# Kernel tuning notes

Hardware: AMD Instinct MI355X
Metric: run time of the kernel (lower is better)

Reference implementation:

```python
import jax, jax.numpy as jnp
import numpy as np

D = 1024

def setup_inputs() -> dict:
    key = jax.random.key(0)
    kx, kw = jax.random.split(key)
    x = jax.random.normal(kx, (4, 2048, D), dtype=jnp.float32)
    # nn.Linear(d, 3d, bias=False): weight [3d, d]; y = x @ W.T
    W = jax.random.normal(kw, (3 * D, D), dtype=jnp.float32) * (1.0 / np.sqrt(D))
    return {"x": x, "W": W}

def reference(x, W):
    d = x.shape[-1]
    qkv = jnp.einsum('bsd,ed->bse', x, W)  # [B,S,3d]
    q, k, v = jnp.split(qkv, 3, axis=2)
    att = jnp.einsum('bqd,bkd->bqk', q, k) * (1.0 / jnp.sqrt(jnp.asarray(d, x.dtype)))
    att = jax.nn.softmax(att, axis=-1)
    y = jnp.einsum('bqk,bkd->bqd', att, v)
    return y
```

## Files before the change

kernel.cpp:

```cpp
#include <hip/hip_runtime.h>
#include <hip/hip_bf16.h>

typedef __attribute__((ext_vector_type(8))) short short8;
typedef __attribute__((ext_vector_type(4))) float f32x4;

typedef unsigned short u16;

__device__ __forceinline__ u16 f32_to_bf16(float f) {
    unsigned int u = __float_as_uint(f);
    u += 0x7fffu + ((u >> 16) & 1u);
    return (u16)(u >> 16);
}

__device__ __forceinline__ void gload16(const u16* g, u16* lds_base) {
    __builtin_amdgcn_global_load_lds(
        (const __attribute__((address_space(1))) void*)g,
        (__attribute__((address_space(3))) void*)lds_base, 16, 0, 0);
}

__global__ void cast_inputs(const float* __restrict__ x, u16* __restrict__ Xb,
                            const float* __restrict__ W, u16* __restrict__ Wb,
                            int nx4, int nw4) {
    int i = blockIdx.x * blockDim.x + threadIdx.x;
    const float* in; u16* out; int idx;
    if (i < nx4) { in = x; out = Xb; idx = i; }
    else { idx = i - nx4; if (idx >= nw4) return; in = W; out = Wb; }
    float4 v = ((const float4*)in)[idx];
    ushort4 o;
    o.x = f32_to_bf16(v.x); o.y = f32_to_bf16(v.y);
    o.z = f32_to_bf16(v.z); o.w = f32_to_bf16(v.w);
    ((ushort4*)out)[idx] = o;
}


struct Frag128 { f32x4 acc[4][4]; int lane, wm, wn; };

__device__ __forceinline__ void gemm_core_128(
    const u16* __restrict__ A, const u16* __restrict__ Bt, int K, int lda, int ldb,
    int row0, int col0, u16* sA, u16* sB, Frag128& fr)
{
    const int t    = threadIdx.x;
    const int lane = t & 63;
    const int wave = t >> 6;
    fr.lane = lane;
    fr.wm = (wave >> 1) * 64;
    fr.wn = (wave & 1) * 64;
    const int lr = lane & 15;

#pragma unroll
    for (int i = 0; i < 4; ++i)
#pragma unroll
        for (int j = 0; j < 4; ++j)
            fr.acc[i][j] = (f32x4){0.f, 0.f, 0.f, 0.f};

    const int srow = lane >> 3;
    const int gc   = (lane & 7) ^ srow;
    for (int k0 = 0; k0 < K; k0 += 64) {
        __syncthreads();
#pragma unroll
        for (int c = 0; c < 4; ++c) {
            const int rb = c * 32 + wave * 8;
            const int r  = rb + srow;
            gload16(A  + (long long)(row0 + r) * lda + k0 + gc * 8, &sA[rb * 64]);
            gload16(Bt + (long long)(col0 + r) * ldb + k0 + gc * 8, &sB[rb * 64]);
        }
        __syncthreads();

#pragma unroll
        for (int kk = 0; kk < 64; kk += 32) {
            const int cb = (lane >> 4) + (kk >> 3);
            const int sl = (cb ^ (lr & 7)) * 8;
            short8 af[4], bf[4];
#pragma unroll
            for (int i = 0; i < 4; ++i) {
                af[i] = *(const short8*)(&sA[(fr.wm + i * 16 + lr) * 64 + sl]);
                bf[i] = *(const short8*)(&sB[(fr.wn + i * 16 + lr) * 64 + sl]);
            }
#pragma unroll
            for (int i = 0; i < 4; ++i)
#pragma unroll
                for (int j = 0; j < 4; ++j)
                    fr.acc[i][j] = __builtin_amdgcn_mfma_f32_16x16x32_bf16(
                        af[i], bf[j], fr.acc[i][j], 0, 0, 0);
        }
    }
}

struct FragN64 { f32x4 acc[2][4]; int lane, wm; };

__device__ __forceinline__ void gemm_core_n64(
    const u16* __restrict__ A, const u16* __restrict__ Bt, int K, int lda, int ldb,
    int row0, int col0, u16* sA, u16* sB, FragN64& fr)
{
    const int t    = threadIdx.x;
    const int lane = t & 63;
    const int wave = t >> 6;
    fr.lane = lane;
    fr.wm = wave * 32;
    const int lr = lane & 15;

#pragma unroll
    for (int i = 0; i < 2; ++i)
#pragma unroll
        for (int j = 0; j < 4; ++j)
            fr.acc[i][j] = (f32x4){0.f, 0.f, 0.f, 0.f};

    const int srow = lane >> 3;
    const int gc   = (lane & 7) ^ srow;
    for (int k0 = 0; k0 < K; k0 += 64) {
        __syncthreads();
#pragma unroll
        for (int c = 0; c < 4; ++c) {
            const int rb = c * 32 + wave * 8;
            gload16(A + (long long)(row0 + rb + srow) * lda + k0 + gc * 8,
                    &sA[rb * 64]);
        }
#pragma unroll
        for (int c = 0; c < 2; ++c) {
            const int rb = c * 32 + wave * 8;
            gload16(Bt + (long long)(col0 + rb + srow) * ldb + k0 + gc * 8,
                    &sB[rb * 64]);
        }
        __syncthreads();

#pragma unroll
        for (int kk = 0; kk < 64; kk += 32) {
            const int cb = (lane >> 4) + (kk >> 3);
            const int sl = (cb ^ (lr & 7)) * 8;
            short8 af[2], bf[4];
#pragma unroll
            for (int i = 0; i < 2; ++i)
                af[i] = *(const short8*)(&sA[(fr.wm + i * 16 + lr) * 64 + sl]);
#pragma unroll
            for (int j = 0; j < 4; ++j)
                bf[j] = *(const short8*)(&sB[(j * 16 + lr) * 64 + sl]);
#pragma unroll
            for (int i = 0; i < 2; ++i)
#pragma unroll
                for (int j = 0; j < 4; ++j)
                    fr.acc[i][j] = __builtin_amdgcn_mfma_f32_16x16x32_bf16(
                        af[i], bf[j], fr.acc[i][j], 0, 0, 0);
        }
    }
}


__global__ __launch_bounds__(256) void gemm_qkv(
    const u16* __restrict__ Xb, const u16* __restrict__ Wb,
    u16* __restrict__ QK, u16* __restrict__ VT)
{
    __shared__ u16 smem[2 * 128 * 64];
    u16* sA = smem;
    u16* sB = smem + 128 * 64;
    const int row0 = blockIdx.y * 128;

    if (blockIdx.x < 16) {
        const int col0 = blockIdx.x * 128;
        Frag128 fr;
        gemm_core_128(Xb, Wb, 1024, 1024, 1024, row0, col0, sA, sB, fr);
        const int cr = (fr.lane >> 4) * 4, cc = fr.lane & 15;
#pragma unroll
        for (int i = 0; i < 4; ++i)
#pragma unroll
            for (int j = 0; j < 4; ++j)
#pragma unroll
                for (int r = 0; r < 4; ++r) {
                    int grow = row0 + fr.wm + i * 16 + cr + r;
                    int gcol = col0 + fr.wn + j * 16 + cc;
                    QK[(long long)grow * 2048 + gcol] = f32_to_bf16(fr.acc[i][j][r]);
                }
    } else {
        const int col0 = (blockIdx.x - 16) * 64;
        FragN64 fr;
        gemm_core_n64(Xb, Wb + 2048 * 1024, 1024, 1024, 1024, row0, col0,
                      sA, sB, fr);
        const int cr = (fr.lane >> 4) * 4, cc = fr.lane & 15;
#pragma unroll
        for (int i = 0; i < 2; ++i) {
            int grow = row0 + fr.wm + i * 16 + cr;
            int b = grow >> 11, s = grow & 2047;
#pragma unroll
            for (int j = 0; j < 4; ++j) {
                int d = col0 + j * 16 + cc;
                ushort4 o;
                o.x = f32_to_bf16(fr.acc[i][j][0]);
                o.y = f32_to_bf16(fr.acc[i][j][1]);
                o.z = f32_to_bf16(fr.acc[i][j][2]);
                o.w = f32_to_bf16(fr.acc[i][j][3]);
                *(ushort4*)(&VT[((long long)(b * 1024 + d)) * 2048 + s]) = o;
            }
        }
    }
}

__global__ __launch_bounds__(256) void gemm_s_exp(
    const u16* __restrict__ QK, u16* __restrict__ E, float* __restrict__ l)
{
    __shared__ u16 sA[128 * 64];
    __shared__ u16 sB[128 * 64];
    const long long boff = (long long)blockIdx.z * 2048 * 2048;
    const u16* Q  = QK + boff;
    const u16* Kp = QK + boff + 1024;
    u16* Eb = E + boff;
    float* lb = l + (long long)blockIdx.z * 2048;
    const int row0 = blockIdx.y * 128;
    const int col0 = blockIdx.x * 128;
    Frag128 fr;
    gemm_core_128(Q, Kp, 1024, 2048, 2048, row0, col0, sA, sB, fr);

    const int cr = (fr.lane >> 4) * 4, cc = fr.lane & 15;
#pragma unroll
    for (int i = 0; i < 4; ++i) {
        float rs[4] = {0.f, 0.f, 0.f, 0.f};
#pragma unroll
        for (int j = 0; j < 4; ++j)
#pragma unroll
            for (int r = 0; r < 4; ++r) {
                float e = __expf(fr.acc[i][j][r] * 0.03125f);
                rs[r] += e;
                int grow = row0 + fr.wm + i * 16 + cr + r;
                int gcol = col0 + fr.wn + j * 16 + cc;
                Eb[(long long)grow * 2048 + gcol] = f32_to_bf16(e);
            }
#pragma unroll
        for (int r = 0; r < 4; ++r) {
#pragma unroll
            for (int m = 1; m < 16; m <<= 1) rs[r] += __shfl_xor(rs[r], m, 64);
            if ((fr.lane & 15) == 0)
                atomicAdd(&lb[row0 + fr.wm + i * 16 + cr + r], rs[r]);
        }
    }
}

__global__ __launch_bounds__(256) void gemm_pv_ts(
    const u16* __restrict__ E, const u16* __restrict__ VT,
    const float* __restrict__ l, float* __restrict__ Y)
{
    __shared__ u16 sA[128 * 64];
    __shared__ u16 sB[128 * 64];
    const u16* VTb = VT + (long long)blockIdx.z * 1024 * 2048;
    const u16* Eb  = E  + (long long)blockIdx.z * 2048 * 2048;
    const float* lb = l + (long long)blockIdx.z * 2048;
    float* Yb = Y + (long long)blockIdx.z * 2048 * 1024;
    const int row0 = blockIdx.y * 128;
    const int col0 = blockIdx.x * 128;
    Frag128 fr;
    gemm_core_128(VTb, Eb, 2048, 2048, 2048, row0, col0, sA, sB, fr);
    const int cr = (fr.lane >> 4) * 4, cc = fr.lane & 15;
#pragma unroll
    for (int j = 0; j < 4; ++j) {
        int q = col0 + fr.wn + j * 16 + cc;
        float inv = 1.0f / lb[q];
#pragma unroll
        for (int i = 0; i < 4; ++i) {
            int d = row0 + fr.wm + i * 16 + cr;
            float4 o = {fr.acc[i][j][0] * inv, fr.acc[i][j][1] * inv,
                        fr.acc[i][j][2] * inv, fr.acc[i][j][3] * inv};
            *(float4*)(&Yb[(long long)q * 1024 + d]) = o;
        }
    }
}

extern "C" void kernel_launch(void* const* d_in, const int* in_sizes, int n_in,
                              void* d_out, int out_size, void* d_ws, size_t ws_size,
                              hipStream_t stream) {
    const float* x = (const float*)d_in[0];
    const float* W = (const float*)d_in[1];
    float* out = (float*)d_out;

    char* ws = (char*)d_ws;
    u16*   Xb = (u16*)(ws);
    u16*   Wb = (u16*)(ws + 16777216LL);
    u16*   QK = (u16*)(ws + 23068672LL);
    u16*   VT = (u16*)(ws + 56623104LL);
    u16*   E  = (u16*)(ws + 73400320LL);
    float* l  = (float*)(ws + 106954752LL);

    hipMemsetAsync(l, 0, 8192 * sizeof(float), stream);

    cast_inputs<<<11264, 256, 0, stream>>>(x, Xb, W, Wb,
                                           8192 * 1024 / 4, 3072 * 1024 / 4);
    gemm_qkv<<<dim3(32, 64, 1), 256, 0, stream>>>(Xb, Wb, QK, VT);
    gemm_s_exp<<<dim3(16, 16, 4), 256, 0, stream>>>(QK, E, l);
    gemm_pv_ts<<<dim3(16, 8, 4), 256, 0, stream>>>(E, VT, l, out);
}
```

Baseline: 257.0 us.

## Use 256x256 double-buffered ping-pong GEMM core for QKV and score kernels

Replaces the 128x128 single-buffered GEMM core in the QKV projection and the QK^T+exp kernels with a 256x256-tile, 8-wave core. The new core double-buffers K-tiles in LDS and interleaves LDS reads, async global-to-LDS loads and MFMA quarter-blocks between explicit barriers, with raised wave priority around the MFMA groups. The aim is to overlap memory traffic with matrix math and raise arithmetic intensity per tile. The cost is 128KB of LDS per block, so only one block fits per CU, fewer blocks in the grid, and heavy barrier use.

```diff
diff --git a/kernel.cpp b/kernel.cpp
--- a/kernel.cpp
+++ b/kernel.cpp
@@ -16,6 +16,19 @@
     __builtin_amdgcn_global_load_lds(
         (const __attribute__((address_space(1))) void*)g,
         (__attribute__((address_space(3))) void*)lds_base, 16, 0, 0);
+}
+
+__device__ __forceinline__ void phase_bar() {
+    __builtin_amdgcn_s_barrier();
+    __builtin_amdgcn_sched_barrier(0);
+}
+__device__ __forceinline__ void wait_vm8() {
+    asm volatile("s_waitcnt vmcnt(8)" ::: "memory");
+    __builtin_amdgcn_sched_barrier(0);
+}
+__device__ __forceinline__ void wait_vm0() {
+    asm volatile("s_waitcnt vmcnt(0)" ::: "memory");
+    __builtin_amdgcn_sched_barrier(0);
 }
 
 __global__ void cast_inputs(const float* __restrict__ x, u16* __restrict__ Xb,
@@ -33,6 +46,249 @@
 }
 
 
+struct Acc256 { f32x4 acc[8][4]; };
+
+template<int MH>
+__device__ __forceinline__ void rd_a(const u16* __restrict__ sA, int wr, int lane,
+                                     int lr, short8 (&af)[4][2]) {
+#pragma unroll
+    for (int a2 = 0; a2 < 4; ++a2) {
+        const int row = wr * 128 + MH * 64 + a2 * 16 + lr;
+#pragma unroll
+        for (int k2 = 0; k2 < 2; ++k2) {
+            const int cb = (lane >> 4) + k2 * 4;
+            af[a2][k2] = *(const short8*)(sA + row * 64 + ((cb ^ (lr & 7)) * 8));
+        }
+    }
+}
+
+template<int NH>
+__device__ __forceinline__ void rd_b(const u16* __restrict__ sB, int wc, int lane,
+                                     int lr, short8 (&bf)[2][2]) {
+#pragma unroll
+    for (int b2 = 0; b2 < 2; ++b2) {
+        const int row = wc * 64 + NH * 32 + b2 * 16 + lr;
+#pragma unroll
+        for (int k2 = 0; k2 < 2; ++k2) {
+            const int cb = (lane >> 4) + k2 * 4;
+            bf[b2][k2] = *(const short8*)(sB + row * 64 + ((cb ^ (lr & 7)) * 8));
+        }
+    }
+}
+
+template<int MH, int NH>
+__device__ __forceinline__ void mm_q(Acc256& fr, const short8 (&af)[4][2],
+                                     const short8 (&bf)[2][2]) {
+    __builtin_amdgcn_s_setprio(1);
+#pragma unroll
+    for (int a2 = 0; a2 < 4; ++a2)
+#pragma unroll
+        for (int b2 = 0; b2 < 2; ++b2)
+#pragma unroll
+            for (int k2 = 0; k2 < 2; ++k2)
+                fr.acc[MH * 4 + a2][NH * 2 + b2] =
+                    __builtin_amdgcn_mfma_f32_16x16x32_bf16(
+                        af[a2][k2], bf[b2][k2],
+                        fr.acc[MH * 4 + a2][NH * 2 + b2], 0, 0, 0);
+    __builtin_amdgcn_s_setprio(0);
+}
+
+__device__ __forceinline__ void gemm_core_256(
+    const u16* __restrict__ A, const u16* __restrict__ Bt,
+    int K, int lda, int ldb, int row0, int col0, u16* sm, Acc256& fr)
+{
+    const int t    = threadIdx.x;
+    const int lane = t & 63;
+    const int wave = t >> 6;
+    const int wr   = wave >> 2;
+    const int wc   = wave & 3;
+    const int lr   = lane & 15;
+    const int srow = lane >> 3;
+    const int gc   = (lane & 7) ^ srow;
+
+    const u16* const sA0 = sm;
+    const u16* const sA1 = sm + 16384;
+    const u16* const sB0 = sm + 32768;
+    const u16* const sB1 = sm + 49152;
+
+#pragma unroll
+    for (int a = 0; a < 8; ++a)
+#pragma unroll
+        for (int b = 0; b < 4; ++b)
+            fr.acc[a][b] = (f32x4){0.f, 0.f, 0.f, 0.f};
+
+    const u16* aB = A  + (long long)(row0 + wave * 8 + srow) * lda + gc * 8;
+    const u16* bB = Bt + (long long)(col0 + wave * 8 + srow) * ldb + gc * 8;
+    u16* const sAw = sm + wave * 512;
+    u16* const sBw = sm + 32768 + wave * 512;
+
+    auto stageA = [&](int kt) {
+        u16* d = sAw + (kt & 1) * 16384;
+        const u16* g = aB + kt * 64;
+#pragma unroll
+        for (int r4 = 0; r4 < 4; ++r4)
+            gload16(g + (long long)(r4 * 64) * lda, d + r4 * 4096);
+    };
+    auto stageB = [&](int kt) {
+        u16* d = sBw + (kt & 1) * 16384;
+        const u16* g = bB + kt * 64;
+#pragma unroll
+        for (int r4 = 0; r4 < 4; ++r4)
+            gload16(g + (long long)(r4 * 64) * ldb, d + r4 * 4096);
+    };
+
+    stageA(0); stageB(0); stageA(1); stageB(1);
+    wait_vm8();
+    phase_bar();
+
+    const int NI = K >> 7;
+    short8 af[4][2], bfa[2][2], bfb[2][2];
+#pragma unroll 1
+    for (int i = 0; i < NI; ++i) {
+        const bool more = (i + 1 < NI);
+        const int t2 = 2 * i + 2;
+
+        rd_a<0>(sA0, wr, lane, lr, af);
+        rd_b<0>(sB0, wc, lane, lr, bfa);
+        phase_bar();
+        mm_q<0, 0>(fr, af, bfa);
+        phase_bar();
+
+        rd_b<1>(sB0, wc, lane, lr, bfb);
+        phase_bar();
+        mm_q<0, 1>(fr, af, bfb);
+        phase_bar();
+
+        rd_a<1>(sA0, wr, lane, lr, af);
+        if (more) stageB(t2);
+        phase_bar();
+        mm_q<1, 1>(fr, af, bfb);
+        phase_bar();
+
+        if (more) stageA(t2);
+        phase_bar();
+        mm_q<1, 0>(fr, af, bfa);
+        if (more) wait_vm8(); else wait_vm0();
+        phase_bar();
+
+        rd_a<0>(sA1, wr, lane, lr, af);
+        rd_b<0>(sB1, wc, lane, lr, bfa);
+        phase_bar();
+        mm_q<0, 0>(fr, af, bfa);
+        phase_bar();
+
+        rd_b<1>(sB1, wc, lane, lr, bfb);
+        phase_bar();
+        mm_q<0, 1>(fr, af, bfb);
+        phase_bar();
+
+        rd_a<1>(sA1, wr, lane, lr, af);
+        if (more) stageB(t2 + 1);
+        phase_bar();
+        mm_q<1, 1>(fr, af, bfb);
+        phase_bar();
+
+        if (more) stageA(t2 + 1);
+        phase_bar();
+        mm_q<1, 0>(fr, af, bfa);
+        if (more) wait_vm8();
+        phase_bar();
+    }
+}
+
+
+__global__ __launch_bounds__(512, 1) void gemm_qkv(
+    const u16* __restrict__ Xb, const u16* __restrict__ Wb,
+    u16* __restrict__ QK, u16* __restrict__ VT)
+{
+    __shared__ u16 sm[65536];
+    const int row0 = blockIdx.y * 256;
+    const bool isV = blockIdx.x >= 8;
+    const int col0 = (isV ? (blockIdx.x - 8) : blockIdx.x) * 256;
+    const u16* Bp  = isV ? (Wb + 2048 * 1024) : Wb;
+
+    Acc256 fr;
+    gemm_core_256(Xb, Bp, 1024, 1024, 1024, row0, col0, sm, fr);
+
+    const int lane = threadIdx.x & 63;
+    const int wave = threadIdx.x >> 6;
+    const int wr = wave >> 2, wc = wave & 3;
+    const int cr = (lane >> 4) * 4, cc = lane & 15;
+
+    if (!isV) {
+#pragma unroll
+        for (int a = 0; a < 8; ++a)
+#pragma unroll
+            for (int b = 0; b < 4; ++b)
+#pragma unroll
+                for (int r = 0; r < 4; ++r) {
+                    int grow = row0 + wr * 128 + a * 16 + cr + r;
+                    int gcol = col0 + wc * 64 + b * 16 + cc;
+                    QK[(long long)grow * 2048 + gcol] = f32_to_bf16(fr.acc[a][b][r]);
+                }
+    } else {
+#pragma unroll
+        for (int a = 0; a < 8; ++a) {
+            int grow = row0 + wr * 128 + a * 16 + cr;
+            int bz = grow >> 11, s = grow & 2047;
+#pragma unroll
+            for (int b = 0; b < 4; ++b) {
+                int d = col0 + wc * 64 + b * 16 + cc;
+                ushort4 o;
+                o.x = f32_to_bf16(fr.acc[a][b][0]);
+                o.y = f32_to_bf16(fr.acc[a][b][1]);
+                o.z = f32_to_bf16(fr.acc[a][b][2]);
+                o.w = f32_to_bf16(fr.acc[a][b][3]);
+                *(ushort4*)(&VT[((long long)(bz * 1024 + d)) * 2048 + s]) = o;
+            }
+        }
+    }
+}
+
+__global__ __launch_bounds__(512, 1) void gemm_s_exp(
+    const u16* __restrict__ QK, u16* __restrict__ E, float* __restrict__ l)
+{
+    __shared__ u16 sm[65536];
+    const long long boff = (long long)blockIdx.z * 2048 * 2048;
+    const u16* Q  = QK + boff;
+    const u16* Kp = QK + boff + 1024;
+    u16* Eb = E + boff;
+    float* lb = l + (long long)blockIdx.z * 2048;
+    const int row0 = blockIdx.y * 256;
+    const int col0 = blockIdx.x * 256;
+
+    Acc256 fr;
+    gemm_core_256(Q, Kp, 1024, 2048, 2048, row0, col0, sm, fr);
+
+    const int lane = threadIdx.x & 63;
+    const int wave = threadIdx.x >> 6;
+    const int wr = wave >> 2, wc = wave & 3;
+    const int cr = (lane >> 4) * 4, cc = lane & 15;
+
+#pragma unroll
+    for (int a = 0; a < 8; ++a) {
+        float rs[4] = {0.f, 0.f, 0.f, 0.f};
+#pragma unroll
+        for (int b = 0; b < 4; ++b)
+#pragma unroll
+            for (int r = 0; r < 4; ++r) {
+                float e = __expf(fr.acc[a][b][r] * 0.03125f);
+                rs[r] += e;
+                int grow = row0 + wr * 128 + a * 16 + cr + r;
+                int gcol = col0 + wc * 64 + b * 16 + cc;
+                Eb[(long long)grow * 2048 + gcol] = f32_to_bf16(e);
+            }
+#pragma unroll
+        for (int r = 0; r < 4; ++r) {
+#pragma unroll
+            for (int m = 1; m < 16; m <<= 1) rs[r] += __shfl_xor(rs[r], m, 64);
+            if ((lane & 15) == 0)
+                atomicAdd(&lb[row0 + wr * 128 + a * 16 + cr + r], rs[r]);
+        }
+    }
+}
+
+
 struct Frag128 { f32x4 acc[4][4]; int lane, wm, wn; };
 
 __device__ __forceinline__ void gemm_core_128(
@@ -82,152 +338,6 @@
                 for (int j = 0; j < 4; ++j)
                     fr.acc[i][j] = __builtin_amdgcn_mfma_f32_16x16x32_bf16(
                         af[i], bf[j], fr.acc[i][j], 0, 0, 0);
-        }
-    }
-}
-
-struct FragN64 { f32x4 acc[2][4]; int lane, wm; };
-
-__device__ __forceinline__ void gemm_core_n64(
-    const u16* __restrict__ A, const u16* __restrict__ Bt, int K, int lda, int ldb,
-    int row0, int col0, u16* sA, u16* sB, FragN64& fr)
-{
-    const int t    = threadIdx.x;
-    const int lane = t & 63;
-    const int wave = t >> 6;
-    fr.lane = lane;
-    fr.wm = wave * 32;
-    const int lr = lane & 15;
-
-#pragma unroll
-    for (int i = 0; i < 2; ++i)
-#pragma unroll
-        for (int j = 0; j < 4; ++j)
-            fr.acc[i][j] = (f32x4){0.f, 0.f, 0.f, 0.f};
-
-    const int srow = lane >> 3;
-    const int gc   = (lane & 7) ^ srow;
-    for (int k0 = 0; k0 < K; k0 += 64) {
-        __syncthreads();
-#pragma unroll
-        for (int c = 0; c < 4; ++c) {
-            const int rb = c * 32 + wave * 8;
-            gload16(A + (long long)(row0 + rb + srow) * lda + k0 + gc * 8,
-                    &sA[rb * 64]);
-        }
-#pragma unroll
-        for (int c = 0; c < 2; ++c) {
-            const int rb = c * 32 + wave * 8;
-            gload16(Bt + (long long)(col0 + rb + srow) * ldb + k0 + gc * 8,
-                    &sB[rb * 64]);
-        }
-        __syncthreads();
-
-#pragma unroll
-        for (int kk = 0; kk < 64; kk += 32) {
-            const int cb = (lane >> 4) + (kk >> 3);
-            const int sl = (cb ^ (lr & 7)) * 8;
-            short8 af[2], bf[4];
-#pragma unroll
-            for (int i = 0; i < 2; ++i)
-                af[i] = *(const short8*)(&sA[(fr.wm + i * 16 + lr) * 64 + sl]);
-#pragma unroll
-            for (int j = 0; j < 4; ++j)
-                bf[j] = *(const short8*)(&sB[(j * 16 + lr) * 64 + sl]);
-#pragma unroll
-            for (int i = 0; i < 2; ++i)
-#pragma unroll
-                for (int j = 0; j < 4; ++j)
-                    fr.acc[i][j] = __builtin_amdgcn_mfma_f32_16x16x32_bf16(
-                        af[i], bf[j], fr.acc[i][j], 0, 0, 0);
-        }
-    }
-}
-
-
-__global__ __launch_bounds__(256) void gemm_qkv(
-    const u16* __restrict__ Xb, const u16* __restrict__ Wb,
-    u16* __restrict__ QK, u16* __restrict__ VT)
-{
-    __shared__ u16 smem[2 * 128 * 64];
-    u16* sA = smem;
-    u16* sB = smem + 128 * 64;
-    const int row0 = blockIdx.y * 128;
-
-    if (blockIdx.x < 16) {
-        const int col0 = blockIdx.x * 128;
-        Frag128 fr;
-        gemm_core_128(Xb, Wb, 1024, 1024, 1024, row0, col0, sA, sB, fr);
-        const int cr = (fr.lane >> 4) * 4, cc = fr.lane & 15;
-#pragma unroll
-        for (int i = 0; i < 4; ++i)
-#pragma unroll
-            for (int j = 0; j < 4; ++j)
-#pragma unroll
-                for (int r = 0; r < 4; ++r) {
-                    int grow = row0 + fr.wm + i * 16 + cr + r;
-                    int gcol = col0 + fr.wn + j * 16 + cc;
-                    QK[(long long)grow * 2048 + gcol] = f32_to_bf16(fr.acc[i][j][r]);
-                }
-    } else {
-        const int col0 = (blockIdx.x - 16) * 64;
-        FragN64 fr;
-        gemm_core_n64(Xb, Wb + 2048 * 1024, 1024, 1024, 1024, row0, col0,
-                      sA, sB, fr);
-        const int cr = (fr.lane >> 4) * 4, cc = fr.lane & 15;
-#pragma unroll
-        for (int i = 0; i < 2; ++i) {
-            int grow = row0 + fr.wm + i * 16 + cr;
-            int b = grow >> 11, s = grow & 2047;
-#pragma unroll
-            for (int j = 0; j < 4; ++j) {
-                int d = col0 + j * 16 + cc;
-                ushort4 o;
-                o.x = f32_to_bf16(fr.acc[i][j][0]);
-                o.y = f32_to_bf16(fr.acc[i][j][1]);
-                o.z = f32_to_bf16(fr.acc[i][j][2]);
-                o.w = f32_to_bf16(fr.acc[i][j][3]);
-                *(ushort4*)(&VT[((long long)(b * 1024 + d)) * 2048 + s]) = o;
-            }
-        }
-    }
-}
-
-__global__ __launch_bounds__(256) void gemm_s_exp(
-    const u16* __restrict__ QK, u16* __restrict__ E, float* __restrict__ l)
-{
-    __shared__ u16 sA[128 * 64];
-    __shared__ u16 sB[128 * 64];
-    const long long boff = (long long)blockIdx.z * 2048 * 2048;
-    const u16* Q  = QK + boff;
-    const u16* Kp = QK + boff + 1024;
-    u16* Eb = E + boff;
-    float* lb = l + (long long)blockIdx.z * 2048;
-    const int row0 = blockIdx.y * 128;
-    const int col0 = blockIdx.x * 128;
-    Frag128 fr;
-    gemm_core_128(Q, Kp, 1024, 2048, 2048, row0, col0, sA, sB, fr);
-
-    const int cr = (fr.lane >> 4) * 4, cc = fr.lane & 15;
-#pragma unroll
-    for (int i = 0; i < 4; ++i) {
-        float rs[4] = {0.f, 0.f, 0.f, 0.f};
-#pragma unroll
-        for (int j = 0; j < 4; ++j)
-#pragma unroll
-            for (int r = 0; r < 4; ++r) {
-                float e = __expf(fr.acc[i][j][r] * 0.03125f);
-                rs[r] += e;
-                int grow = row0 + fr.wm + i * 16 + cr + r;
-                int gcol = col0 + fr.wn + j * 16 + cc;
-                Eb[(long long)grow * 2048 + gcol] = f32_to_bf16(e);
-            }
-#pragma unroll
-        for (int r = 0; r < 4; ++r) {
-#pragma unroll
-            for (int m = 1; m < 16; m <<= 1) rs[r] += __shfl_xor(rs[r], m, 64);
-            if ((fr.lane & 15) == 0)
-                atomicAdd(&lb[row0 + fr.wm + i * 16 + cr + r], rs[r]);
         }
     }
 }
@@ -280,7 +390,7 @@
 
     cast_inputs<<<11264, 256, 0, stream>>>(x, Xb, W, Wb,
                                            8192 * 1024 / 4, 3072 * 1024 / 4);
-    gemm_qkv<<<dim3(32, 64, 1), 256, 0, stream>>>(Xb, Wb, QK, VT);
-    gemm_s_exp<<<dim3(16, 16, 4), 256, 0, stream>>>(QK, E, l);
+    gemm_qkv<<<dim3(12, 32, 1), 512, 0, stream>>>(Xb, Wb, QK, VT);
+    gemm_s_exp<<<dim3(8, 8, 4), 512, 0, stream>>>(QK, E, l);
     gemm_pv_ts<<<dim3(16, 8, 4), 256, 0, stream>>>(E, VT, l, out);
 }
```

Result: faster. 243.4 us (-5.3%).
